# Optimization experiments

Hardware: AMD Instinct MI355X
Metric: run time of the kernel (lower is better)

Reference implementation:

```python
import jax, jax.numpy as jnp
import numpy as np
import math

D_MODEL = 768
N_HEADS = 12
B, L = 2, 2048
ALPHA = 0.3

def setup_inputs() -> dict:
    key = jax.random.key(0)
    ks = jax.random.split(key, 7)
    s = 0.02
    return {
        "x": jax.random.normal(ks[0], (B, L, D_MODEL), dtype=jnp.float32),
        "Wqkv_w": jax.random.normal(ks[1], (D_MODEL, 3 * D_MODEL), dtype=jnp.float32) * s,
        "Wqkv_b": jax.random.normal(ks[2], (3 * D_MODEL,), dtype=jnp.float32) * s,
        "sel_w": jax.random.normal(ks[3], (D_MODEL, 2), dtype=jnp.float32) * s,
        "sel_b": jax.random.normal(ks[4], (2,), dtype=jnp.float32) * s,
        "out_w": jax.random.normal(ks[5], (D_MODEL, D_MODEL), dtype=jnp.float32) * s,
        "out_b": jax.random.normal(ks[6], (D_MODEL,), dtype=jnp.float32) * s,
        "temperature": jnp.ones((1,), dtype=jnp.float32) * (math.sqrt(D_MODEL) * ALPHA),
    }

def reference(x, Wqkv_w, Wqkv_b, sel_w, sel_b, out_w, out_b, temperature):
    b, l, d = x.shape
    h = N_HEADS
    hd = d // h
    # QKV projection: (B, L, 3, H, hd)
    qkv = (x @ Wqkv_w + Wqkv_b).reshape(b, l, 3, h, hd)
    q, k_, v = qkv[:, :, 0], qkv[:, :, 1], qkv[:, :, 2]
    scale = 1.0 / math.sqrt(hd)
    scores = jnp.einsum('bthd,bshd->bhts', q, k_ * scale)  # (B,H,L,L)
    causal_mask = jnp.triu(jnp.full((l, l), -10000.0, dtype=scores.dtype), 1)
    attn = jax.nn.softmax(scores + causal_mask, axis=-1)
    ctx = jnp.einsum('bhts,bshd->bthd', attn, v).reshape(b, l, d)
    attn_output = ctx @ out_w + out_b  # (B,L,D)
    # selection gate: softmax over 2 logits, keep prob of class 1 -> (B,L,1)
    selection = jax.nn.softmax((x @ sel_w + sel_b) / temperature, axis=-1)[..., 1:]
    # eval-mode top-k routing
    k_sel = int(math.ceil(math.sqrt(l)))
    _, idx = jax.lax.top_k(selection[..., 0], k_sel)  # (B, k)
    gated = attn_output * selection  # (B,L,D)
    src = jnp.take_along_axis(gated, idx[..., None], axis=1)  # (B,k,D)
    y = jax.vmap(lambda xb, ib, sb: xb.at[ib].add(sb))(x, idx, src)
    return y
```

## Files before the change

kernel.cpp:

```cpp
#include <hip/hip_runtime.h>
#include <hip/hip_bf16.h>
#include <cstddef>

#define BATCH 2
#define SEQ   2048
#define DM    768
#define NH    12
#define HD    64
#define N3    2304
#define NKV   1536
#define KSEL  46
#define NROW  (BATCH*KSEL)
#define NCHUNK 32

typedef unsigned short ushort_t;
typedef __attribute__((ext_vector_type(8))) short bf16x8;
typedef __attribute__((ext_vector_type(4))) float f32x4;

__device__ __forceinline__ ushort_t f2bf(float f) {
  union { __hip_bfloat16 h; ushort_t u; } cv;
  cv.h = __float2bfloat16(f);
  return cv.u;
}
__device__ __forceinline__ float bf2f(ushort_t u) {
  union { unsigned int i; float f; } cv;
  cv.i = ((unsigned int)u) << 16;
  return cv.f;
}

#define GLD16(g, l)                                                         \
  __builtin_amdgcn_global_load_lds(                                         \
      (const __attribute__((address_space(1))) void*)(g),                   \
      (__attribute__((address_space(3))) void*)(l), 16, 0, 0)

__global__ __launch_bounds__(256) void prep_kernel(
    const float* __restrict__ x, const float* __restrict__ W,
    const float* __restrict__ Wo,
    const float* __restrict__ sel_w, const float* __restrict__ sel_b,
    const float* __restrict__ temp,
    ushort_t* __restrict__ xb, ushort_t* __restrict__ Wt,
    ushort_t* __restrict__ WoT,
    float* __restrict__ sel, float* __restrict__ y) {
  const int bx = blockIdx.x;
  const int tid = threadIdx.x;
  if (bx < 1024) {
    const int w = tid >> 6, lane = tid & 63;
    const int row = bx * 4 + w;
    const float4* xr4 = (const float4*)(x + (size_t)row * DM);
    float4* yr4 = (float4*)(y + (size_t)row * DM);
    ushort4* xb4 = (ushort4*)(xb + (size_t)row * DM);
    const float4* sw4 = (const float4*)sel_w;
    float a0 = 0.f, a1 = 0.f;
#pragma unroll
    for (int i = 0; i < 3; ++i) {
      const int p = i * 64 + lane;
      float4 f = xr4[p];
      yr4[p] = f;
      ushort4 o;
      o.x = f2bf(f.x); o.y = f2bf(f.y); o.z = f2bf(f.z); o.w = f2bf(f.w);
      xb4[p] = o;
      float4 sa = sw4[p * 2];
      float4 sb = sw4[p * 2 + 1];
      a0 += f.x * sa.x + f.y * sa.z + f.z * sb.x + f.w * sb.z;
      a1 += f.x * sa.y + f.y * sa.w + f.z * sb.y + f.w * sb.w;
    }
    for (int off = 32; off; off >>= 1) {
      a0 += __shfl_xor(a0, off);
      a1 += __shfl_xor(a1, off);
    }
    if (lane == 0) {
      float t = temp[0];
      float l0 = (a0 + sel_b[0]) / t;
      float l1 = (a1 + sel_b[1]) / t;
      sel[row] = 1.0f / (1.0f + expf(l0 - l1));
    }
  } else if (bx < 2752) {
    __shared__ float tile[32][33];
    const int bx2 = bx - 1024;
    const int n0 = (bx2 % 72) * 32, k0 = (bx2 / 72) * 32;
    const int r = tid >> 3, c4 = (tid & 7) * 4;
    float4 f = *(const float4*)&W[(size_t)(k0 + r) * N3 + n0 + c4];
    tile[r][c4] = f.x; tile[r][c4 + 1] = f.y; tile[r][c4 + 2] = f.z; tile[r][c4 + 3] = f.w;
    __syncthreads();
    ushort4 o;
    o.x = f2bf(tile[c4 + 0][r]);
    o.y = f2bf(tile[c4 + 1][r]);
    o.z = f2bf(tile[c4 + 2][r]);
    o.w = f2bf(tile[c4 + 3][r]);
    *(ushort4*)&Wt[(size_t)(n0 + r) * DM + k0 + c4] = o;
  } else {
    __shared__ float tile2[32][33];
    const int bx3 = bx - 2752;
    const int n0 = (bx3 % 24) * 32, k0 = (bx3 / 24) * 32;
    const int r = tid >> 3, c4 = (tid & 7) * 4;
    float4 f = *(const float4*)&Wo[(size_t)(k0 + r) * DM + n0 + c4];
    tile2[r][c4] = f.x; tile2[r][c4 + 1] = f.y; tile2[r][c4 + 2] = f.z; tile2[r][c4 + 3] = f.w;
    __syncthreads();
    ushort4 o;
    o.x = f2bf(tile2[c4 + 0][r]);
    o.y = f2bf(tile2[c4 + 1][r]);
    o.z = f2bf(tile2[c4 + 2][r]);
    o.w = f2bf(tile2[c4 + 3][r]);
    *(ushort4*)&WoT[(size_t)(n0 + r) * DM + k0 + c4] = o;
  }
}

__global__ __launch_bounds__(256) void topk_kernel(
    const float* __restrict__ sel, int* __restrict__ idx,
    int* __restrict__ idxp) {
  __shared__ unsigned int hist[256];
  __shared__ unsigned int cum[256];
  __shared__ unsigned int wtot[4];
  __shared__ int sh_b;
  __shared__ int c_gt, c_eq;
  __shared__ int tmp_gt[KSEL];
  __shared__ int eqlist[256];
  __shared__ int fin[64];
  __shared__ int srt[64];
  const int b = blockIdx.x, tid = threadIdx.x;
  const int lane = tid & 63, w = tid >> 6;

  unsigned int key[8];
  int  kidx[8];
#pragma unroll
  for (int e = 0; e < 8; ++e) {
    int i = e * 256 + tid;
    kidx[e] = i;
    key[e] = __float_as_uint(sel[b * SEQ + i]);
  }
  unsigned int prefix = 0, mask = 0;
  int r = KSEL;
#pragma unroll
  for (int p = 3; p >= 0; --p) {
    const int shift = 8 * p;
    hist[tid] = 0;
    __syncthreads();
#pragma unroll
    for (int e = 0; e < 8; ++e)
      if ((key[e] & mask) == prefix)
        atomicAdd(&hist[(key[e] >> shift) & 255], 1u);
    __syncthreads();
    unsigned int v = hist[tid];
#pragma unroll
    for (int off = 1; off < 64; off <<= 1) {
      unsigned int t = __shfl_down(v, off);
      if (lane + off < 64) v += t;
    }
    if (lane == 0) wtot[w] = v;
    __syncthreads();
    unsigned int addhi = 0;
    for (int ww = w + 1; ww < 4; ++ww) addhi += wtot[ww];
    v += addhi;
    cum[tid] = v;
    __syncthreads();
    if (v >= (unsigned int)r && (tid == 255 || cum[tid + 1] < (unsigned int)r))
      sh_b = tid;
    __syncthreads();
    const int bsel = sh_b;
    r -= (bsel == 255) ? 0 : (int)cum[bsel + 1];
    prefix |= ((unsigned int)bsel) << shift;
    mask |= 0xFFu << shift;
    __syncthreads();
  }
  if (tid == 0) { c_gt = 0; c_eq = 0; }
  __syncthreads();
#pragma unroll
  for (int e = 0; e < 8; ++e) {
    if (key[e] > prefix) {
      int pos = atomicAdd(&c_gt, 1);
      tmp_gt[pos] = kidx[e];
    } else if (key[e] == prefix) {
      int pos = atomicAdd(&c_eq, 1);
      if (pos < 256) eqlist[pos] = kidx[e];
    }
  }
  __syncthreads();
  if (tid == 0) {
    const int need = KSEL - c_gt;
    const int ec = (c_eq < 256) ? c_eq : 256;
    for (int a = 0; a < need; ++a) {
      int mb = a;
      for (int bb = a + 1; bb < ec; ++bb)
        if (eqlist[bb] < eqlist[mb]) mb = bb;
      int tv = eqlist[a]; eqlist[a] = eqlist[mb]; eqlist[mb] = tv;
    }
  }
  __syncthreads();
  if (tid < KSEL)
    fin[tid] = (tid < c_gt) ? tmp_gt[tid] : eqlist[tid - c_gt];
  __syncthreads();
  if (tid < KSEL) {
    const int v = fin[tid];
    int rank = 0;
    for (int j = 0; j < KSEL; ++j) rank += (fin[j] < v);
    srt[rank] = v;
  }
  __syncthreads();
  if (tid < 64) {
    if (tid < KSEL) {
      idx[b * KSEL + tid] = srt[tid];
      idxp[b * 64 + tid] = srt[tid];
    } else {
      idxp[b * 64 + tid] = 0;
    }
  }
}

__global__ __launch_bounds__(256) void gemm_kernel(
    const ushort_t* __restrict__ Xbf,
    const ushort_t* __restrict__ Wt,
    const float* __restrict__ bias,
    const int* __restrict__ idxp,
    ushort_t* __restrict__ Ckv,
    ushort_t* __restrict__ qb) {
  __shared__ ushort_t As[128 * 64];
  __shared__ ushort_t Bs[128 * 64];
  const int bid = blockIdx.x;
  const int tid = threadIdx.x;
  const int lane = tid & 63, w = tid >> 6;
  const int wr = w >> 1, wc = w & 1;
  const int quad = lane >> 4, l16 = lane & 15;
  const bool isQ = (bid >= 384);
  int m0, n0;
  int srow[4], scol[4];
#pragma unroll
  for (int j = 0; j < 4; ++j) {
    const int chunk = (j * 4 + w) * 64 + lane;
    srow[j] = chunk >> 3;
    scol[j] = ((chunk & 7) ^ (srow[j] & 7)) * 8;
  }
  size_t gaRow[4], gbRow[4];
  if (isQ) {
    m0 = 0;
    n0 = (bid - 384) * 128;
#pragma unroll
    for (int j = 0; j < 4; ++j)
      gaRow[j] = (size_t)((srow[j] >> 6) * SEQ + idxp[srow[j]]) * DM;
  } else {
    const int bid2 = (bid & 7) * 48 + (bid >> 3);
    m0 = (bid2 / 12) * 128;
    n0 = 768 + (bid2 % 12) * 128;
#pragma unroll
    for (int j = 0; j < 4; ++j)
      gaRow[j] = (size_t)(m0 + srow[j]) * DM;
  }
#pragma unroll
  for (int j = 0; j < 4; ++j)
    gbRow[j] = (size_t)(n0 + srow[j]) * DM;

  f32x4 acc[4][4] = {};
  for (int k0 = 0; k0 < DM; k0 += 64) {
#pragma unroll
    for (int j = 0; j < 4; ++j) {
      GLD16(Xbf + gaRow[j] + k0 + scol[j], &As[(j * 4 + w) * 512]);
      GLD16(Wt + gbRow[j] + k0 + scol[j], &Bs[(j * 4 + w) * 512]);
    }
    __syncthreads();
    bf16x8 af[4][2], bfr[4][2];
#pragma unroll
    for (int i = 0; i < 4; ++i) {
      const int row = wr * 64 + i * 16 + l16;
      const int sw = row & 7;
#pragma unroll
      for (int ks = 0; ks < 2; ++ks)
        af[i][ks] = *(const bf16x8*)&As[row * 64 + (((quad + ks * 4) ^ sw) * 8)];
    }
#pragma unroll
    for (int j2 = 0; j2 < 4; ++j2) {
      const int row = wc * 64 + j2 * 16 + l16;
      const int sw = row & 7;
#pragma unroll
      for (int ks = 0; ks < 2; ++ks)
        bfr[j2][ks] = *(const bf16x8*)&Bs[row * 64 + (((quad + ks * 4) ^ sw) * 8)];
    }
#pragma unroll
    for (int i = 0; i < 4; ++i)
#pragma unroll
      for (int j2 = 0; j2 < 4; ++j2) {
        acc[i][j2] = __builtin_amdgcn_mfma_f32_16x16x32_bf16(af[i][0], bfr[j2][0], acc[i][j2], 0, 0, 0);
        acc[i][j2] = __builtin_amdgcn_mfma_f32_16x16x32_bf16(af[i][1], bfr[j2][1], acc[i][j2], 0, 0, 0);
      }
    __syncthreads();
  }
#pragma unroll
  for (int i = 0; i < 4; ++i) {
    const int row_base = wr * 64 + i * 16 + quad * 4;
#pragma unroll
    for (int j = 0; j < 4; ++j) {
      const int col = n0 + wc * 64 + j * 16 + l16;
      const float bv = bias[col];
      if (isQ) {
#pragma unroll
        for (int r = 0; r < 4; ++r)
          qb[(size_t)(row_base + r) * DM + col] = f2bf(acc[i][j][r] + bv);
      } else {
#pragma unroll
        for (int r = 0; r < 4; ++r)
          Ckv[(size_t)(m0 + row_base + r) * NKV + (col - 768)] = f2bf(acc[i][j][r] + bv);
      }
    }
  }
}

__global__ __launch_bounds__(256) void attn_chunk_kernel(
    const ushort_t* __restrict__ kv,
    const ushort_t* __restrict__ qb,
    const int* __restrict__ idx,
    float* __restrict__ m_part, float* __restrict__ l_part,
    ushort_t* __restrict__ o_part) {
  __shared__ __align__(16) ushort_t Vt[64][72];
  __shared__ __align__(16) ushort_t Ps[4][16][72];
  __shared__ int tS[64];
  __shared__ int tmaxS;
  const int tid = threadIdx.x;
  const int c = blockIdx.x, h = blockIdx.y, b = blockIdx.z;
  const int c0 = c * 64;
  if (tid < 64) {
    int t = (tid < KSEL) ? idx[b * KSEL + tid] : -1;
    tS[tid] = t;
    int tm = t;
    for (int off = 32; off; off >>= 1) tm = max(tm, __shfl_xor(tm, off));
    if (tid == 0) tmaxS = tm;
  }
  __syncthreads();
  if (c0 > tmaxS) return;

  {
    const int key = tid >> 2, ds0 = (tid & 3) * 16;
    const ushort_t* vsrc = kv + (size_t)(b * SEQ + c0 + key) * NKV + DM + h * HD + ds0;
    ushort_t tmp[16];
    *(uint4*)&tmp[0] = *(const uint4*)&vsrc[0];
    *(uint4*)&tmp[8] = *(const uint4*)&vsrc[8];
#pragma unroll
    for (int i = 0; i < 16; ++i) Vt[ds0 + i][key] = tmp[i];
  }

  const int lane = tid & 63, w = tid >> 6;
  const int quad = lane >> 4, l16 = lane & 15;

  const ushort_t* qsrc = qb + (size_t)(b * 64 + w * 16 + l16) * DM + h * HD + quad * 8;
  bf16x8 aq0 = *(const bf16x8*)&qsrc[0];
  bf16x8 aq1 = *(const bf16x8*)&qsrc[32];

  f32x4 acc[4] = {};
#pragma unroll
  for (int nt = 0; nt < 4; ++nt) {
    const ushort_t* ksrc = kv + (size_t)(b * SEQ + c0 + nt * 16 + l16) * NKV + h * HD + quad * 8;
    bf16x8 bk0 = *(const bf16x8*)&ksrc[0];
    bf16x8 bk1 = *(const bf16x8*)&ksrc[32];
    acc[nt] = __builtin_amdgcn_mfma_f32_16x16x32_bf16(aq0, bk0, acc[nt], 0, 0, 0);
    acc[nt] = __builtin_amdgcn_mfma_f32_16x16x32_bf16(aq1, bk1, acc[nt], 0, 0, 0);
  }

  float p[4][4];
  float mrow[4], lrow[4];
#pragma unroll
  for (int r = 0; r < 4; ++r) {
    const int q = w * 16 + quad * 4 + r;
    const int t = tS[q];
    float mx = -1e30f;
#pragma unroll
    for (int nt = 0; nt < 4; ++nt) {
      float s = acc[nt][r] * 0.125f;
      if (c0 + nt * 16 + l16 > t) s = -1e30f;
      p[nt][r] = s;
      mx = fmaxf(mx, s);
    }
#pragma unroll
    for (int off = 1; off < 16; off <<= 1) mx = fmaxf(mx, __shfl_xor(mx, off));
    float sum = 0.f;
#pragma unroll
    for (int nt = 0; nt < 4; ++nt) {
      float pv = __expf(p[nt][r] - mx);
      p[nt][r] = pv;
      sum += pv;
    }
#pragma unroll
    for (int off = 1; off < 16; off <<= 1) sum += __shfl_xor(sum, off);
    mrow[r] = mx; lrow[r] = sum;
  }

  const size_t pbase = ((size_t)(b * NH + h) * NCHUNK + c) * 64;
  if (l16 == 0) {
#pragma unroll
    for (int r = 0; r < 4; ++r) {
      const int q = w * 16 + quad * 4 + r;
      m_part[pbase + q] = mrow[r];
      l_part[pbase + q] = lrow[r];
    }
  }

#pragma unroll
  for (int r = 0; r < 4; ++r)
#pragma unroll
    for (int nt = 0; nt < 4; ++nt)
      Ps[w][quad * 4 + r][nt * 16 + l16] = f2bf(p[nt][r]);
  __syncthreads();

  bf16x8 ap0 = *(const bf16x8*)&Ps[w][l16][quad * 8];
  bf16x8 ap1 = *(const bf16x8*)&Ps[w][l16][32 + quad * 8];
  f32x4 acc2[4] = {};
#pragma unroll
  for (int nt = 0; nt < 4; ++nt) {
    bf16x8 bv0 = *(const bf16x8*)&Vt[nt * 16 + l16][quad * 8];
    bf16x8 bv1 = *(const bf16x8*)&Vt[nt * 16 + l16][32 + quad * 8];
    acc2[nt] = __builtin_amdgcn_mfma_f32_16x16x32_bf16(ap0, bv0, acc2[nt], 0, 0, 0);
    acc2[nt] = __builtin_amdgcn_mfma_f32_16x16x32_bf16(ap1, bv1, acc2[nt], 0, 0, 0);
  }
  ushort_t* obp = o_part + pbase * 64;
#pragma unroll
  for (int nt = 0; nt < 4; ++nt)
#pragma unroll
    for (int r = 0; r < 4; ++r)
      obp[(w * 16 + quad * 4 + r) * 64 + nt * 16 + l16] = f2bf(acc2[nt][r]);
}

__global__ __launch_bounds__(256) void attn_combine_kernel(
    const float* __restrict__ m_part, const float* __restrict__ l_part,
    const ushort_t* __restrict__ o_part, const int* __restrict__ idx,
    ushort_t* __restrict__ ctx_bf) {
  __shared__ float wgt[NCHUNK][16];
  __shared__ float linv[16];
  __shared__ int ncS[16];
  const int rg = blockIdx.x, h = blockIdx.y, b = blockIdx.z;
  const int tid = threadIdx.x;
  const size_t base = (size_t)(b * NH + h) * NCHUNK * 64;
  if (tid < 16) {
    const int q = rg * 16 + tid;
    float L = 0.f; int nc = 0;
    if (q < KSEL) {
      const int t = idx[b * KSEL + q];
      nc = (t >> 6) + 1;
      float M = -1e30f;
      for (int cc = 0; cc < nc; ++cc)
        M = fmaxf(M, m_part[base + cc * 64 + q]);
      for (int cc = 0; cc < nc; ++cc) {
        float wv = __expf(m_part[base + cc * 64 + q] - M);
        wgt[cc][tid] = wv;
        L += wv * l_part[base + cc * 64 + q];
      }
    }
    ncS[tid] = nc;
    linv[tid] = (L > 0.f) ? 1.0f / L : 0.f;
  }
  __syncthreads();
  const int rl = tid >> 4;
  const int d4 = (tid & 15) * 4;
  const int q = rg * 16 + rl;
  if (q >= KSEL) return;
  const int nc = ncS[rl];
  float4 a = {0.f, 0.f, 0.f, 0.f};
  const ushort_t* obp = o_part + base * 64 + (size_t)q * 64 + d4;
  for (int cc = 0; cc < nc; ++cc) {
    const float wv = wgt[cc][rl];
    const ushort4 ov = *(const ushort4*)&obp[(size_t)cc * 4096];
    a.x += wv * bf2f(ov.x); a.y += wv * bf2f(ov.y);
    a.z += wv * bf2f(ov.z); a.w += wv * bf2f(ov.w);
  }
  const float li = linv[rl];
  ushort4 o;
  o.x = f2bf(a.x * li); o.y = f2bf(a.y * li);
  o.z = f2bf(a.z * li); o.w = f2bf(a.w * li);
  *(ushort4*)&ctx_bf[(size_t)(b * 64 + q) * DM + h * HD + d4] = o;
}

__global__ __launch_bounds__(256) void outproj_kernel(
    const ushort_t* __restrict__ ctx_bf,
    const ushort_t* __restrict__ WoT,
    const float* __restrict__ ob, const int* __restrict__ idx,
    const float* __restrict__ sel, float* __restrict__ y) {
  __shared__ ushort_t As[128 * 128];
  __shared__ ushort_t Bs[64 * 128];
  const int tid = threadIdx.x;
  const int lane = tid & 63, w = tid >> 6;
  const int wr = w >> 1, wc = w & 1;
  const int kb = blockIdx.x / 12;
  const int n0 = (blockIdx.x % 12) * 64;
  const int kbase = kb * 384;
  const int quad = lane >> 4, l16 = lane & 15;
  int srA[8], scA[8], srB[4], scB[4];
#pragma unroll
  for (int j = 0; j < 8; ++j) {
    const int chunk = (j * 4 + w) * 64 + lane;
    srA[j] = chunk >> 4;
    const int ci = chunk & 15;
    scA[j] = ((ci & 8) | ((ci & 7) ^ (srA[j] & 7))) * 8;
  }
#pragma unroll
  for (int j = 0; j < 4; ++j) {
    const int chunk = (j * 4 + w) * 64 + lane;
    srB[j] = chunk >> 4;
    const int ci = chunk & 15;
    scB[j] = ((ci & 8) | ((ci & 7) ^ (srB[j] & 7))) * 8;
  }
  f32x4 acc[4][2] = {};
  for (int k0 = kbase; k0 < kbase + 384; k0 += 128) {
#pragma unroll
    for (int j = 0; j < 8; ++j)
      GLD16(ctx_bf + (size_t)srA[j] * DM + k0 + scA[j], &As[(j * 4 + w) * 512]);
#pragma unroll
    for (int j = 0; j < 4; ++j)
      GLD16(WoT + (size_t)(n0 + srB[j]) * DM + k0 + scB[j], &Bs[(j * 4 + w) * 512]);
    __syncthreads();
    bf16x8 af[4][4], bfr[2][4];
#pragma unroll
    for (int i = 0; i < 4; ++i) {
      const int row = wr * 64 + i * 16 + l16;
      const int sw = row & 7;
#pragma unroll
      for (int ks = 0; ks < 4; ++ks) {
        const int ci = quad + ks * 4;
        af[i][ks] = *(const bf16x8*)&As[row * 128 + (((ci & 8) | ((ci & 7) ^ sw)) * 8)];
      }
    }
#pragma unroll
    for (int j = 0; j < 2; ++j) {
      const int row = wc * 32 + j * 16 + l16;
      const int sw = row & 7;
#pragma unroll
      for (int ks = 0; ks < 4; ++ks) {
        const int ci = quad + ks * 4;
        bfr[j][ks] = *(const bf16x8*)&Bs[row * 128 + (((ci & 8) | ((ci & 7) ^ sw)) * 8)];
      }
    }
#pragma unroll
    for (int i = 0; i < 4; ++i)
#pragma unroll
      for (int j = 0; j < 2; ++j)
#pragma unroll
        for (int ks = 0; ks < 4; ++ks)
          acc[i][j] = __builtin_amdgcn_mfma_f32_16x16x32_bf16(af[i][ks], bfr[j][ks], acc[i][j], 0, 0, 0);
    __syncthreads();
  }
#pragma unroll
  for (int i = 0; i < 4; ++i) {
#pragma unroll
    for (int r = 0; r < 4; ++r) {
      const int row = wr * 64 + i * 16 + quad * 4 + r;
      const int b = row >> 6, jj = row & 63;
      if (jj >= KSEL) continue;
      const int t = idx[b * KSEL + jj];
      const float sv = sel[b * SEQ + t];
      float* yr = y + (size_t)(b * SEQ + t) * DM;
#pragma unroll
      for (int j = 0; j < 2; ++j) {
        const int col = n0 + wc * 32 + j * 16 + l16;
        const float bv = (kb == 0) ? ob[col] : 0.f;
        atomicAdd(&yr[col], (acc[i][j][r] + bv) * sv);
      }
    }
  }
}

extern "C" void kernel_launch(void* const* d_in, const int* in_sizes, int n_in,
                              void* d_out, int out_size, void* d_ws, size_t ws_size,
                              hipStream_t stream) {
  const float* x      = (const float*)d_in[0];
  const float* Wqkv_w = (const float*)d_in[1];
  const float* Wqkv_b = (const float*)d_in[2];
  const float* sel_w  = (const float*)d_in[3];
  const float* sel_b  = (const float*)d_in[4];
  const float* out_w  = (const float*)d_in[5];
  const float* out_b  = (const float*)d_in[6];
  const float* temp   = (const float*)d_in[7];
  float* y = (float*)d_out;

  char* wsb = (char*)d_ws;
  ushort_t* kv     = (ushort_t*)wsb;  wsb += (size_t)BATCH * SEQ * NKV * 2;
  ushort_t* o_part = (ushort_t*)wsb;  wsb += (size_t)24 * NCHUNK * 64 * 64 * 2;
  float*    m_part = (float*)wsb;     wsb += (size_t)24 * NCHUNK * 64 * 4;
  float*    l_part = (float*)wsb;     wsb += (size_t)24 * NCHUNK * 64 * 4;
  float*    sel    = (float*)wsb;     wsb += (size_t)BATCH * SEQ * 4;
  int*      idx    = (int*)wsb;       wsb += 128 * 4;
  int*      idxp   = (int*)wsb;       wsb += 128 * 4;
  ushort_t* ctx_bf = (ushort_t*)wsb;  wsb += (size_t)128 * DM * 2;
  ushort_t* qb     = (ushort_t*)wsb;  wsb += (size_t)128 * DM * 2;
  ushort_t* Xbf    = (ushort_t*)wsb;  wsb += (size_t)BATCH * SEQ * DM * 2;
  ushort_t* Wt     = (ushort_t*)wsb;  wsb += (size_t)N3 * DM * 2;
  ushort_t* WoT    = (ushort_t*)wsb;  wsb += (size_t)DM * DM * 2;

  prep_kernel<<<dim3(3328), 256, 0, stream>>>(x, Wqkv_w, out_w, sel_w, sel_b, temp,
                                              Xbf, Wt, WoT, sel, y);
  topk_kernel<<<dim3(BATCH), 256, 0, stream>>>(sel, idx, idxp);
  gemm_kernel<<<dim3(390), 256, 0, stream>>>(Xbf, Wt, Wqkv_b, idxp, kv, qb);
  attn_chunk_kernel<<<dim3(NCHUNK, NH, BATCH), 256, 0, stream>>>(kv, qb, idx, m_part, l_part, o_part);
  attn_combine_kernel<<<dim3(3, NH, BATCH), 256, 0, stream>>>(m_part, l_part, o_part, idx, ctx_bf);
  outproj_kernel<<<dim3(6 * 4), 256, 0, stream>>>(ctx_bf, WoT, out_b, idx, sel, y);
}
```

Before: 152.2 us.

## Fuse top-k selection into QKV GEMM kernel with flag-based inter-block sync

The separate top-k kernel launch is removed and its work runs in two extra blocks of the GEMM kernel. The Q-projection blocks spin on global flags until those blocks publish the selected indices, then stage them in shared memory. The K/V GEMM blocks do not depend on top-k, so they run alongside it and one launch gap is removed. The cost is spin-waiting blocks and a reliance on the top-k blocks being scheduled, which holds here because they come before the Q blocks in the grid.

Result: no change. 153.2 us (+0.7%).

```diff
diff --git a/kernel.cpp b/kernel.cpp
--- a/kernel.cpp
+++ b/kernel.cpp
@@ -40,10 +40,12 @@
     const float* __restrict__ temp,
     ushort_t* __restrict__ xb, ushort_t* __restrict__ Wt,
     ushort_t* __restrict__ WoT,
-    float* __restrict__ sel, float* __restrict__ y) {
+    float* __restrict__ sel, float* __restrict__ y,
+    unsigned int* __restrict__ flag) {
   const int bx = blockIdx.x;
   const int tid = threadIdx.x;
   if (bx < 1024) {
+    if (bx == 0 && tid < 2) flag[tid] = 0u;
     const int w = tid >> 6, lane = tid & 63;
     const int row = bx * 4 + w;
     const float4* xr4 = (const float4*)(x + (size_t)row * DM);
@@ -105,122 +107,129 @@
   }
 }
 
-__global__ __launch_bounds__(256) void topk_kernel(
-    const float* __restrict__ sel, int* __restrict__ idx,
-    int* __restrict__ idxp) {
-  __shared__ unsigned int hist[256];
-  __shared__ unsigned int cum[256];
-  __shared__ unsigned int wtot[4];
-  __shared__ int sh_b;
-  __shared__ int c_gt, c_eq;
-  __shared__ int tmp_gt[KSEL];
-  __shared__ int eqlist[256];
-  __shared__ int fin[64];
-  __shared__ int srt[64];
-  const int b = blockIdx.x, tid = threadIdx.x;
-  const int lane = tid & 63, w = tid >> 6;
-
-  unsigned int key[8];
-  int  kidx[8];
-#pragma unroll
-  for (int e = 0; e < 8; ++e) {
-    int i = e * 256 + tid;
-    kidx[e] = i;
-    key[e] = __float_as_uint(sel[b * SEQ + i]);
-  }
-  unsigned int prefix = 0, mask = 0;
-  int r = KSEL;
-#pragma unroll
-  for (int p = 3; p >= 0; --p) {
-    const int shift = 8 * p;
-    hist[tid] = 0;
-    __syncthreads();
-#pragma unroll
-    for (int e = 0; e < 8; ++e)
-      if ((key[e] & mask) == prefix)
-        atomicAdd(&hist[(key[e] >> shift) & 255], 1u);
-    __syncthreads();
-    unsigned int v = hist[tid];
-#pragma unroll
-    for (int off = 1; off < 64; off <<= 1) {
-      unsigned int t = __shfl_down(v, off);
-      if (lane + off < 64) v += t;
-    }
-    if (lane == 0) wtot[w] = v;
-    __syncthreads();
-    unsigned int addhi = 0;
-    for (int ww = w + 1; ww < 4; ++ww) addhi += wtot[ww];
-    v += addhi;
-    cum[tid] = v;
-    __syncthreads();
-    if (v >= (unsigned int)r && (tid == 255 || cum[tid + 1] < (unsigned int)r))
-      sh_b = tid;
-    __syncthreads();
-    const int bsel = sh_b;
-    r -= (bsel == 255) ? 0 : (int)cum[bsel + 1];
-    prefix |= ((unsigned int)bsel) << shift;
-    mask |= 0xFFu << shift;
-    __syncthreads();
-  }
-  if (tid == 0) { c_gt = 0; c_eq = 0; }
-  __syncthreads();
-#pragma unroll
-  for (int e = 0; e < 8; ++e) {
-    if (key[e] > prefix) {
-      int pos = atomicAdd(&c_gt, 1);
-      tmp_gt[pos] = kidx[e];
-    } else if (key[e] == prefix) {
-      int pos = atomicAdd(&c_eq, 1);
-      if (pos < 256) eqlist[pos] = kidx[e];
-    }
-  }
-  __syncthreads();
-  if (tid == 0) {
-    const int need = KSEL - c_gt;
-    const int ec = (c_eq < 256) ? c_eq : 256;
-    for (int a = 0; a < need; ++a) {
-      int mb = a;
-      for (int bb = a + 1; bb < ec; ++bb)
-        if (eqlist[bb] < eqlist[mb]) mb = bb;
-      int tv = eqlist[a]; eqlist[a] = eqlist[mb]; eqlist[mb] = tv;
-    }
-  }
-  __syncthreads();
-  if (tid < KSEL)
-    fin[tid] = (tid < c_gt) ? tmp_gt[tid] : eqlist[tid - c_gt];
-  __syncthreads();
-  if (tid < KSEL) {
-    const int v = fin[tid];
-    int rank = 0;
-    for (int j = 0; j < KSEL; ++j) rank += (fin[j] < v);
-    srt[rank] = v;
-  }
-  __syncthreads();
-  if (tid < 64) {
-    if (tid < KSEL) {
-      idx[b * KSEL + tid] = srt[tid];
-      idxp[b * 64 + tid] = srt[tid];
-    } else {
-      idxp[b * 64 + tid] = 0;
-    }
-  }
-}
-
 __global__ __launch_bounds__(256) void gemm_kernel(
     const ushort_t* __restrict__ Xbf,
     const ushort_t* __restrict__ Wt,
     const float* __restrict__ bias,
-    const int* __restrict__ idxp,
+    const float* __restrict__ sel,
+    int* __restrict__ idx,
+    int* __restrict__ idxp,
+    unsigned int* __restrict__ flag,
     ushort_t* __restrict__ Ckv,
     ushort_t* __restrict__ qb) {
   __shared__ ushort_t As[128 * 64];
   __shared__ ushort_t Bs[128 * 64];
+  __shared__ int idxp_s[128];
   const int bid = blockIdx.x;
   const int tid = threadIdx.x;
   const int lane = tid & 63, w = tid >> 6;
+
+  if (bid == 384 || bid == 385) {
+    __shared__ unsigned int hist[256];
+    __shared__ unsigned int cum[256];
+    __shared__ unsigned int wtot[4];
+    __shared__ int sh_b;
+    __shared__ int c_gt, c_eq;
+    __shared__ int tmp_gt[KSEL];
+    __shared__ int eqlist[256];
+    __shared__ int fin[64];
+    __shared__ int srt[64];
+    const int b = bid - 384;
+    unsigned int key[8];
+    int kidx[8];
+#pragma unroll
+    for (int e = 0; e < 8; ++e) {
+      int i = e * 256 + tid;
+      kidx[e] = i;
+      key[e] = __float_as_uint(sel[b * SEQ + i]);
+    }
+    unsigned int prefix = 0, mask = 0;
+    int r = KSEL;
+#pragma unroll
+    for (int p = 3; p >= 0; --p) {
+      const int shift = 8 * p;
+      hist[tid] = 0;
+      __syncthreads();
+#pragma unroll
+      for (int e = 0; e < 8; ++e)
+        if ((key[e] & mask) == prefix)
+          atomicAdd(&hist[(key[e] >> shift) & 255], 1u);
+      __syncthreads();
+      unsigned int v = hist[tid];
+#pragma unroll
+      for (int off = 1; off < 64; off <<= 1) {
+        unsigned int t = __shfl_down(v, off);
+        if (lane + off < 64) v += t;
+      }
+      if (lane == 0) wtot[w] = v;
+      __syncthreads();
+      unsigned int addhi = 0;
+      for (int ww = w + 1; ww < 4; ++ww) addhi += wtot[ww];
+      v += addhi;
+      cum[tid] = v;
+      __syncthreads();
+      if (v >= (unsigned int)r && (tid == 255 || cum[tid + 1] < (unsigned int)r))
+        sh_b = tid;
+      __syncthreads();
+      const int bsel = sh_b;
+      r -= (bsel == 255) ? 0 : (int)cum[bsel + 1];
+      prefix |= ((unsigned int)bsel) << shift;
+      mask |= 0xFFu << shift;
+      __syncthreads();
+    }
+    if (tid == 0) { c_gt = 0; c_eq = 0; }
+    __syncthreads();
+#pragma unroll
+    for (int e = 0; e < 8; ++e) {
+      if (key[e] > prefix) {
+        int pos = atomicAdd(&c_gt, 1);
+        tmp_gt[pos] = kidx[e];
+      } else if (key[e] == prefix) {
+        int pos = atomicAdd(&c_eq, 1);
+        if (pos < 256) eqlist[pos] = kidx[e];
+      }
+    }
+    __syncthreads();
+    if (tid == 0) {
+      const int need = KSEL - c_gt;
+      const int ec = (c_eq < 256) ? c_eq : 256;
+      for (int a = 0; a < need; ++a) {
+        int mb = a;
+        for (int bb = a + 1; bb < ec; ++bb)
+          if (eqlist[bb] < eqlist[mb]) mb = bb;
+        int tv = eqlist[a]; eqlist[a] = eqlist[mb]; eqlist[mb] = tv;
+      }
+    }
+    __syncthreads();
+    if (tid < KSEL)
+      fin[tid] = (tid < c_gt) ? tmp_gt[tid] : eqlist[tid - c_gt];
+    __syncthreads();
+    if (tid < KSEL) {
+      const int v = fin[tid];
+      int rank = 0;
+      for (int j = 0; j < KSEL; ++j) rank += (fin[j] < v);
+      srt[rank] = v;
+    }
+    __syncthreads();
+    if (tid < 64) {
+      if (tid < KSEL) {
+        idx[b * KSEL + tid] = srt[tid];
+        idxp[b * 64 + tid] = srt[tid];
+      } else {
+        idxp[b * 64 + tid] = 0;
+      }
+    }
+    __syncthreads();
+    if (tid == 0) {
+      __threadfence();
+      __hip_atomic_store(&flag[b], 1u, __ATOMIC_RELEASE, __HIP_MEMORY_SCOPE_AGENT);
+    }
+    return;
+  }
+
   const int wr = w >> 1, wc = w & 1;
   const int quad = lane >> 4, l16 = lane & 15;
-  const bool isQ = (bid >= 384);
+  const bool isQ = (bid >= 386);
   int m0, n0;
   int srow[4], scol[4];
 #pragma unroll
@@ -231,11 +240,20 @@
   }
   size_t gaRow[4], gbRow[4];
   if (isQ) {
+    if (tid == 0) {
+      while (__hip_atomic_load(&flag[0], __ATOMIC_ACQUIRE, __HIP_MEMORY_SCOPE_AGENT) == 0u) {}
+      while (__hip_atomic_load(&flag[1], __ATOMIC_ACQUIRE, __HIP_MEMORY_SCOPE_AGENT) == 0u) {}
+    }
+    __syncthreads();
+    if (tid < 128)
+      idxp_s[tid] = (int)__hip_atomic_load((unsigned int*)&idxp[tid],
+                                           __ATOMIC_RELAXED, __HIP_MEMORY_SCOPE_AGENT);
+    __syncthreads();
     m0 = 0;
-    n0 = (bid - 384) * 128;
+    n0 = (bid - 386) * 128;
 #pragma unroll
     for (int j = 0; j < 4; ++j)
-      gaRow[j] = (size_t)((srow[j] >> 6) * SEQ + idxp[srow[j]]) * DM;
+      gaRow[j] = (size_t)((srow[j] >> 6) * SEQ + idxp_s[srow[j]]) * DM;
   } else {
     const int bid2 = (bid & 7) * 48 + (bid >> 3);
     m0 = (bid2 / 12) * 128;
@@ -573,6 +591,7 @@
   float*    sel    = (float*)wsb;     wsb += (size_t)BATCH * SEQ * 4;
   int*      idx    = (int*)wsb;       wsb += 128 * 4;
   int*      idxp   = (int*)wsb;       wsb += 128 * 4;
+  unsigned int* flag = (unsigned int*)wsb; wsb += 128 * 4;
   ushort_t* ctx_bf = (ushort_t*)wsb;  wsb += (size_t)128 * DM * 2;
   ushort_t* qb     = (ushort_t*)wsb;  wsb += (size_t)128 * DM * 2;
   ushort_t* Xbf    = (ushort_t*)wsb;  wsb += (size_t)BATCH * SEQ * DM * 2;
@@ -580,9 +599,8 @@
   ushort_t* WoT    = (ushort_t*)wsb;  wsb += (size_t)DM * DM * 2;
 
   prep_kernel<<<dim3(3328), 256, 0, stream>>>(x, Wqkv_w, out_w, sel_w, sel_b, temp,
-                                              Xbf, Wt, WoT, sel, y);
-  topk_kernel<<<dim3(BATCH), 256, 0, stream>>>(sel, idx, idxp);
-  gemm_kernel<<<dim3(390), 256, 0, stream>>>(Xbf, Wt, Wqkv_b, idxp, kv, qb);
+                                              Xbf, Wt, WoT, sel, y, flag);
+  gemm_kernel<<<dim3(392), 256, 0, stream>>>(Xbf, Wt, Wqkv_b, sel, idx, idxp, flag, kv, qb);
   attn_chunk_kernel<<<dim3(NCHUNK, NH, BATCH), 256, 0, stream>>>(kv, qb, idx, m_part, l_part, o_part);
   attn_combine_kernel<<<dim3(3, NH, BATCH), 256, 0, stream>>>(m_part, l_part, o_part, idx, ctx_bf);
   outproj_kernel<<<dim3(6 * 4), 256, 0, stream>>>(ctx_bf, WoT, out_b, idx, sel, y);
```
